# Optimization experiments

Hardware: AMD Instinct MI355X
Metric: run time of the kernel (lower is better)

## Reference

```python
import jax, jax.numpy as jnp
import numpy as np

N = 100000
E = 1600000
D_IN = 128
D_OUT = 128
D_DEC = 2
TAU = 0.5
NEG_SLOPE = 0.2  # PyG GATv2Conv default negative_slope


def _glorot(key, shape):
    lim = (6.0 / (shape[0] + shape[1])) ** 0.5
    return jax.random.uniform(key, shape, jnp.float32, -lim, lim)


def gatv2(x, edge_index, Wl, Wr, bl, br, att, bias):
    """PyG GATv2Conv, heads=1, add_self_loops=True, eval mode (no dropout).
    out[i] = sum_j softmax_i( att . leaky_relu(xl[j] + xr[i]) ) * xl[j] + bias
    """
    n = x.shape[0]
    loops = jnp.arange(n, dtype=edge_index.dtype)
    src = jnp.concatenate([edge_index[0], loops])  # [E+N]
    dst = jnp.concatenate([edge_index[1], loops])
    xl = x @ Wl + bl  # [N, out]
    xr = x @ Wr + br
    # per-edge unnormalized score
    e = jax.nn.leaky_relu(xl[src] + xr[dst], NEG_SLOPE) @ att  # [E+N]
    # scatter-softmax over incoming edges of each target node
    m = jax.ops.segment_max(e, dst, num_segments=n)
    a = jnp.exp(e - m[dst])
    s = jax.ops.segment_sum(a, dst, num_segments=n)
    alpha = a / (s[dst] + 1e-16)
    out = jax.ops.segment_sum(alpha[:, None] * xl[src], dst, num_segments=n)
    return out + bias


def setup_inputs() -> dict:
    key = jax.random.key(0)
    ks = jax.random.split(key, 16)
    x = jax.random.normal(ks[0], (N, D_IN), jnp.float32)
    edge_dec = jax.random.randint(ks[1], (2, E), 0, N, jnp.int64)
    edge_0 = jax.random.randint(ks[2], (2, E), 0, N, jnp.int64)
    edge_1 = jax.random.randint(ks[3], (2, E), 0, N, jnp.int64)
    u = jax.random.uniform(ks[4], (N, D_DEC), jnp.float32, 1e-6, 1.0 - 1e-6)
    gumbel = -jnp.log(-jnp.log(u))  # Gumbel(0,1) noise
    # shared GAT (used for every decision branch)
    Wl_g = _glorot(ks[5], (D_IN, D_OUT))
    Wr_g = _glorot(ks[6], (D_IN, D_OUT))
    bl_g = jnp.zeros((D_OUT,), jnp.float32)
    br_g = jnp.zeros((D_OUT,), jnp.float32)
    att_g = _glorot(ks[7], (D_OUT, 1))[:, 0]
    bias_g = jnp.zeros((D_OUT,), jnp.float32)
    # decision GAT
    Wl_d = _glorot(ks[8], (D_IN, D_DEC))
    Wr_d = _glorot(ks[9], (D_IN, D_DEC))
    bl_d = jnp.zeros((D_DEC,), jnp.float32)
    br_d = jnp.zeros((D_DEC,), jnp.float32)
    att_d = _glorot(ks[10], (D_DEC, 1))[:, 0]
    bias_d = jnp.zeros((D_DEC,), jnp.float32)
    return {"x": x, "edge_dec": edge_dec, "edge_0": edge_0, "edge_1": edge_1,
            "gumbel": gumbel,
            "Wl_g": Wl_g, "Wr_g": Wr_g, "bl_g": bl_g, "br_g": br_g,
            "att_g": att_g, "bias_g": bias_g,
            "Wl_d": Wl_d, "Wr_d": Wr_d, "bl_d": bl_d, "br_d": br_d,
            "att_d": att_d, "bias_d": bias_d}


def reference(x, edge_dec, edge_0, edge_1, gumbel,
              Wl_g, Wr_g, bl_g, br_g, att_g, bias_g,
              Wl_d, Wr_d, bl_d, br_d, att_d, bias_d):
    # decision logits via decision GAT on the decision edge set
    logits = gatv2(x, edge_dec, Wl_d, Wr_d, bl_d, br_d, att_d, bias_d)  # [N, 2]
    # hard gumbel-softmax with straight-through estimator, tau=0.5
    y_soft = jax.nn.softmax((logits + gumbel) / TAU, axis=-1)
    idx = jnp.argmax(y_soft, axis=-1)
    y_hard = jax.nn.one_hot(idx, y_soft.shape[-1], dtype=y_soft.dtype)
    decisions = y_hard + y_soft - jax.lax.stop_gradient(y_soft)
    # per-decision GAT (shared weights, different edge sets), gated sum
    out = jnp.zeros((x.shape[0], Wl_g.shape[1]), x.dtype)
    for i, ei in enumerate([edge_0, edge_1]):
        out = out + gatv2(x, ei, Wl_g, Wr_g, bl_g, br_g, att_g, bias_g) * decisions[:, i:i + 1]
    return out
```

## Files before the change

kernel.cpp:

```cpp
#include <hip/hip_runtime.h>

#define NEG 0.2f
#define CAPD16 384
#define CAPC16 704
#define CH 9216
#define NT 512
#define CSH 9
#define FPC 32
#define NCMAX 256
#define CHB 512
#define CCAPD 9216
#define CCAPC 17408

typedef __attribute__((ext_vector_type(8))) short short8;
typedef __attribute__((ext_vector_type(4))) float f32x4;

static __device__ __forceinline__ unsigned short f2bf(float f) {
  unsigned u = __float_as_uint(f);
  u += 0x7fffu + ((u >> 16) & 1u);
  return (unsigned short)(u >> 16);
}
static __device__ __forceinline__ float bflo(unsigned u) {
  return __uint_as_float(u << 16);
}
static __device__ __forceinline__ float bfhi(unsigned u) {
  return __uint_as_float(u & 0xffff0000u);
}
static __device__ __forceinline__ float bfx(const uint4& v, int f) {
  unsigned c = (f < 2) ? v.x : (f < 4) ? v.y : (f < 6) ? v.z : v.w;
  return (f & 1) ? bfhi(c) : bflo(c);
}
static __device__ __forceinline__ unsigned f2u(float f) {
  unsigned b = __float_as_uint(f);
  return (b & 0x80000000u) ? ~b : (b | 0x80000000u);
}
static __device__ __forceinline__ float u2f(unsigned u) {
  unsigned b = (u & 0x80000000u) ? (u ^ 0x80000000u) : ~u;
  return __uint_as_float(b);
}

__global__ void k_prep_wt(const float* __restrict__ Wl, const float* __restrict__ Wr,
                          unsigned short* __restrict__ wt, int* __restrict__ gccur,
                          int ncur) {
  if (blockIdx.x < 128) {
    int idx = blockIdx.x * 256 + threadIdx.x;
    int c = idx >> 7, k = idx & 127;
    float v = (c < 128) ? Wl[(size_t)k * 128 + c] : Wr[(size_t)k * 128 + (c - 128)];
    wt[idx] = f2bf(v);
  } else {
    int i = (blockIdx.x - 128) * 256 + threadIdx.x;
    if (i < ncur) gccur[i] = 0;
  }
}

__global__ __launch_bounds__(256) void k_gemm_main(
    const float* __restrict__ x, const unsigned short* __restrict__ wt,
    const float* __restrict__ bl, const float* __restrict__ br,
    const float* __restrict__ Wld, const float* __restrict__ Wrd,
    const float* __restrict__ bld, const float* __restrict__ brd,
    unsigned short* __restrict__ xl, unsigned short* __restrict__ xr,
    float* __restrict__ xld, float* __restrict__ xrd, int N) {
  int w = threadIdx.x >> 6, lane = threadIdx.x & 63;
  int m = lane & 15, quad = lane >> 4;
  int rowbase = blockIdx.x * 16;
  if (rowbase >= N) return;
  int colbase = w * 64;
  f32x4 acc[4] = {};
  float dl0 = 0.f, dl1 = 0.f, dr0 = 0.f, dr1 = 0.f;
  const float* arow = x + (size_t)(rowbase + m) * 128 + quad * 8;
#pragma unroll
  for (int kb = 0; kb < 128; kb += 32) {
    float4 a0 = *(const float4*)(arow + kb);
    float4 a1 = *(const float4*)(arow + kb + 4);
    if (w == 0) {
      int k0 = kb + quad * 8;
      const float4* wl4 = (const float4*)(Wld + 2 * k0);
      const float4* wr4 = (const float4*)(Wrd + 2 * k0);
      float4 l0 = wl4[0], l1 = wl4[1], l2 = wl4[2], l3 = wl4[3];
      float4 r0 = wr4[0], r1 = wr4[1], r2 = wr4[2], r3 = wr4[3];
      dl0 = fmaf(a0.x, l0.x, dl0); dl1 = fmaf(a0.x, l0.y, dl1);
      dl0 = fmaf(a0.y, l0.z, dl0); dl1 = fmaf(a0.y, l0.w, dl1);
      dl0 = fmaf(a0.z, l1.x, dl0); dl1 = fmaf(a0.z, l1.y, dl1);
      dl0 = fmaf(a0.w, l1.z, dl0); dl1 = fmaf(a0.w, l1.w, dl1);
      dl0 = fmaf(a1.x, l2.x, dl0); dl1 = fmaf(a1.x, l2.y, dl1);
      dl0 = fmaf(a1.y, l2.z, dl0); dl1 = fmaf(a1.y, l2.w, dl1);
      dl0 = fmaf(a1.z, l3.x, dl0); dl1 = fmaf(a1.z, l3.y, dl1);
      dl0 = fmaf(a1.w, l3.z, dl0); dl1 = fmaf(a1.w, l3.w, dl1);
      dr0 = fmaf(a0.x, r0.x, dr0); dr1 = fmaf(a0.x, r0.y, dr1);
      dr0 = fmaf(a0.y, r0.z, dr0); dr1 = fmaf(a0.y, r0.w, dr1);
      dr0 = fmaf(a0.z, r1.x, dr0); dr1 = fmaf(a0.z, r1.y, dr1);
      dr0 = fmaf(a0.w, r1.z, dr0); dr1 = fmaf(a0.w, r1.w, dr1);
      dr0 = fmaf(a1.x, r2.x, dr0); dr1 = fmaf(a1.x, r2.y, dr1);
      dr0 = fmaf(a1.y, r2.z, dr0); dr1 = fmaf(a1.y, r2.w, dr1);
      dr0 = fmaf(a1.z, r3.x, dr0); dr1 = fmaf(a1.z, r3.y, dr1);
      dr0 = fmaf(a1.w, r3.z, dr0); dr1 = fmaf(a1.w, r3.w, dr1);
    }
    short8 af;
    af[0] = (short)f2bf(a0.x); af[1] = (short)f2bf(a0.y);
    af[2] = (short)f2bf(a0.z); af[3] = (short)f2bf(a0.w);
    af[4] = (short)f2bf(a1.x); af[5] = (short)f2bf(a1.y);
    af[6] = (short)f2bf(a1.z); af[7] = (short)f2bf(a1.w);
#pragma unroll
    for (int ct = 0; ct < 4; ct++) {
      const unsigned short* bp =
          wt + (size_t)(colbase + ct * 16 + m) * 128 + kb + quad * 8;
      short8 bfr = *(const short8*)bp;
      acc[ct] = __builtin_amdgcn_mfma_f32_16x16x32_bf16(af, bfr, acc[ct], 0, 0, 0);
    }
  }
  if (w == 0) {
    dl0 += __shfl_xor(dl0, 16); dl0 += __shfl_xor(dl0, 32);
    dl1 += __shfl_xor(dl1, 16); dl1 += __shfl_xor(dl1, 32);
    dr0 += __shfl_xor(dr0, 16); dr0 += __shfl_xor(dr0, 32);
    dr1 += __shfl_xor(dr1, 16); dr1 += __shfl_xor(dr1, 32);
    if (quad == 0) {
      int row = rowbase + m;
      float2 vl; vl.x = dl0 + bld[0]; vl.y = dl1 + bld[1];
      float2 vr; vr.x = dr0 + brd[0]; vr.y = dr1 + brd[1];
      *(float2*)(xld + 2 * (size_t)row) = vl;
      *(float2*)(xrd + 2 * (size_t)row) = vr;
    }
  }
#pragma unroll
  for (int ct = 0; ct < 4; ct++) {
    int c = colbase + ct * 16 + m;
    float badd = (c < 128) ? bl[c] : br[c - 128];
#pragma unroll
    for (int r = 0; r < 4; r++) {
      int row = rowbase + quad * 4 + r;
      unsigned short v = f2bf(acc[ct][r] + badd);
      if (c < 128) xl[(size_t)row * 128 + c] = v;
      else         xr[(size_t)row * 128 + (c - 128)] = v;
    }
  }
}

__global__ __launch_bounds__(NT) void k_bin_coarse(
    const int* __restrict__ ed, const int* __restrict__ e0,
    const int* __restrict__ e1, int* __restrict__ gccur,
    unsigned* __restrict__ cbind, unsigned* __restrict__ cbinc,
    long E, int NC) {
  __shared__ unsigned stage[CH];
  __shared__ int h[CHB + 1];
  __shared__ int gbase[CHB];
  __shared__ int wtot[8], wexcl[8];
  int tid = threadIdx.x;
  long base = (long)blockIdx.x * CH;
  long T = 3 * E;
  for (int a = tid; a < CHB + 1; a += NT) h[a] = 0;
  __syncthreads();
  for (int it = 0; it < CH / NT; it++) {
    long idx = base + it * NT + tid;
    if (idx < T) {
      int ha;
      if (idx < E) ha = ed[E + idx] >> CSH;
      else if (idx < 2 * E) ha = NCMAX + (e0[idx] >> CSH);
      else ha = NCMAX + (e1[idx - E] >> CSH);
      atomicAdd(&h[ha], 1);
    }
  }
  __syncthreads();
  {
    int v = h[tid];
    int lane = tid & 63, wv = tid >> 6;
    int inc = v;
    for (int off = 1; off < 64; off <<= 1) {
      int nv = __shfl_up(inc, off);
      if (lane >= off) inc += nv;
    }
    if (lane == 63) wtot[wv] = inc;
    __syncthreads();
    if (tid == 0) {
      int r = 0;
      for (int i = 0; i < 8; i++) { wexcl[i] = r; r += wtot[i]; }
    }
    __syncthreads();
    int excl = wexcl[wv] + inc - v;
    h[tid] = excl;
    if (tid == NT - 1) h[CHB] = excl + v;
  }
  __syncthreads();
  {
    int a = tid;
    int cnt = h[a + 1] - h[a];
    if (cnt > 0) {
      if (a < NCMAX) { if (a < NC) gbase[a] = atomicAdd(&gccur[a], cnt); }
      else { int b = a - NCMAX; if (b < NC) gbase[a] = atomicAdd(&gccur[NC + b], cnt); }
    }
  }
  __syncthreads();
  for (int it = 0; it < CH / NT; it++) {
    long idx = base + it * NT + tid;
    if (idx < T) {
      int ha; unsigned pay;
      if (idx < E) {
        int s = ed[idx], t = ed[E + idx];
        ha = t >> CSH;
        pay = ((unsigned)s << CSH) | (unsigned)(t & ((1 << CSH) - 1));
      } else {
        int k = idx >= 2 * E;
        const int* L = k ? e1 : e0;
        long j = idx - E - (k ? E : 0);
        int s = L[j], t = L[E + j];
        ha = NCMAX + (t >> CSH);
        pay = ((unsigned)s << (CSH + 1)) | ((unsigned)k << CSH) |
              (unsigned)(t & ((1 << CSH) - 1));
      }
      int pos = atomicAdd(&h[ha], 1);
      stage[pos] = pay;
    }
  }
  __syncthreads();
  int lane = tid & 63, wv = tid >> 6;
  for (int a = wv; a < 2 * NCMAX; a += 8) {
    int start = a ? h[a - 1] : 0;
    int end = h[a];
    int len = end - start;
    if (len <= 0) continue;
    int gb = gbase[a];
    if (a < NCMAX) {
      if (a < NC) {
        unsigned* dst = cbind + (size_t)a * CCAPD;
        for (int i = lane; i < len; i += 64) {
          int o = gb + i;
          if (o < CCAPD) dst[o] = stage[start + i];
        }
      }
    } else {
      int b = a - NCMAX;
      if (b < NC) {
        unsigned* dst = cbinc + (size_t)b * CCAPC;
        for (int i = lane; i < len; i += 64) {
          int o = gb + i;
          if (o < CCAPC) dst[o] = stage[start + i];
        }
      }
    }
  }
}

__global__ __launch_bounds__(NT) void k_bin_fine(
    const unsigned* __restrict__ cbind, const unsigned* __restrict__ cbinc,
    const int* __restrict__ gccur, unsigned* __restrict__ bind,
    unsigned* __restrict__ binc, int* __restrict__ cntd, int* __restrict__ cntc,
    int NC, int NB16) {
  __shared__ int cur[FPC];
  int cb = blockIdx.x;
  int isC = cb >= NC;
  int c = isC ? cb - NC : cb;
  int cnt = gccur[cb];
  int ccap = isC ? CCAPC : CCAPD;
  if (cnt > ccap) cnt = ccap;
  const unsigned* src = isC ? (cbinc + (size_t)c * CCAPC)
                            : (cbind + (size_t)c * CCAPD);
  int tid = threadIdx.x;
  if (tid < FPC) cur[tid] = 0;
  __syncthreads();
  if (isC) {
    for (int i = tid; i < cnt; i += NT) {
      unsigned pay = src[i];
      int f = (pay >> 4) & (FPC - 1);
      int fb = c * FPC + f;
      int pos = atomicAdd(&cur[f], 1);
      unsigned o = ((pay >> (CSH + 1)) << 5) | (((pay >> CSH) & 1u) << 4) |
                   (pay & 15u);
      if (pos < CAPC16 && fb < NB16) binc[(size_t)fb * CAPC16 + pos] = o;
    }
  } else {
    for (int i = tid; i < cnt; i += NT) {
      unsigned pay = src[i];
      int f = (pay >> 4) & (FPC - 1);
      int fb = c * FPC + f;
      int pos = atomicAdd(&cur[f], 1);
      unsigned o = ((pay >> CSH) << 4) | (pay & 15u);
      if (pos < CAPD16 && fb < NB16) bind[(size_t)fb * CAPD16 + pos] = o;
    }
  }
  __syncthreads();
  if (tid < FPC) {
    int fb = c * FPC + tid;
    if (fb < NB16) {
      if (isC) { int v = cur[tid]; if (v > CAPC16) v = CAPC16; cntc[fb] = v; }
      else     { int v = cur[tid]; if (v > CAPD16) v = CAPD16; cntd[fb] = v; }
    }
  }
}

__global__ __launch_bounds__(256) void k_fused(
    const unsigned* __restrict__ bind, const unsigned* __restrict__ binc,
    const int* __restrict__ cntd_, const int* __restrict__ cntc_,
    const unsigned short* __restrict__ xl, const unsigned short* __restrict__ xr,
    const float* __restrict__ xld, const float* __restrict__ xrd,
    const float* __restrict__ attd, const float* __restrict__ biasd,
    const float* __restrict__ g, const float* __restrict__ att,
    const float* __restrict__ bias, float* __restrict__ out, int N) {
  __shared__ float xrd_s[32];
  __shared__ unsigned nmax[16];
  __shared__ float nsum[16], na0[16], na1[16];
  __shared__ int dec_s[16], scnt[16];
  __shared__ int slots[16 * 65];
  int tid = threadIdx.x;
  int b = blockIdx.x, nb0 = b << 4;
  int cdn = cntd_[b]; if (cdn > CAPD16) cdn = CAPD16;
  int ccn = cntc_[b]; if (ccn > CAPC16) ccn = CAPC16;
  float a0 = attd[0], a1 = attd[1];
  float eself = 0.f, x0s = 0.f, x1s = 0.f;
  if (tid < 16) {
    int node = nb0 + tid;
    if (node < N) {
      float2 xrv = *(const float2*)(xrd + 2 * (size_t)node);
      xrd_s[2 * tid] = xrv.x; xrd_s[2 * tid + 1] = xrv.y;
      float2 xlv = *(const float2*)(xld + 2 * (size_t)node);
      x0s = xlv.x; x1s = xlv.y;
      float h0 = x0s + xrv.x, h1 = x1s + xrv.y;
      eself = a0 * fmaxf(h0, NEG * h0) + a1 * fmaxf(h1, NEG * h1);
      nmax[tid] = f2u(eself);
    } else {
      xrd_s[2 * tid] = 0.f; xrd_s[2 * tid + 1] = 0.f;
      nmax[tid] = f2u(0.f);
    }
    nsum[tid] = 0.f; na0[tid] = 0.f; na1[tid] = 0.f;
  }
  __syncthreads();
  const unsigned* bd = bind + (size_t)b * CAPD16;
  const float2* xld2 = (const float2*)xld;
  auto dscore = [&](float2 v, int tl) {
    float h0 = v.x + xrd_s[2 * tl], h1 = v.y + xrd_s[2 * tl + 1];
    return a0 * fmaxf(h0, NEG * h0) + a1 * fmaxf(h1, NEG * h1);
  };
  for (int i = tid; i < cdn; i += 256) {
    unsigned pk = bd[i];
    float2 v = xld2[pk >> 4];
    int tl = pk & 15;
    atomicMax(&nmax[tl], f2u(dscore(v, tl)));
  }
  __syncthreads();
  for (int i = tid; i < cdn; i += 256) {
    unsigned pk = bd[i];
    float2 v = xld2[pk >> 4];
    int tl = pk & 15;
    float w = expf(dscore(v, tl) - u2f(nmax[tl]));
    atomicAdd(&nsum[tl], w); atomicAdd(&na0[tl], w * v.x); atomicAdd(&na1[tl], w * v.y);
  }
  __syncthreads();
  if (tid < 16) {
    int node = nb0 + tid;
    if (node < N) {
      float mm = u2f(nmax[tid]);
      float ws = expf(eself - mm);
      float den = nsum[tid] + ws + 1e-16f;
      float z0 = (na0[tid] + ws * x0s) / den + biasd[0] + g[2 * (size_t)node];
      float z1 = (na1[tid] + ws * x1s) / den + biasd[1] + g[2 * (size_t)node + 1];
      dec_s[tid] = (z1 > z0) ? 1 : 0;
      scnt[tid] = 1; slots[tid * 65] = node;
    } else {
      dec_s[tid] = -1; scnt[tid] = 0; slots[tid * 65] = 0;
    }
  }
  __syncthreads();
  const unsigned* bc = binc + (size_t)b * CAPC16;
  for (int i = tid; i < ccn; i += 256) {
    unsigned pk = bc[i];
    int tl = pk & 15, k = (pk >> 4) & 1;
    if (k == dec_s[tl]) {
      int pos = atomicAdd(&scnt[tl], 1);
      if (pos < 64) slots[tl * 65 + pos] = pk >> 5;
    }
  }
  __syncthreads();

  int l = tid & 15, gg = tid >> 4;
  const float4* at4 = (const float4*)att;
  float4 atA = at4[l * 2], atB = at4[l * 2 + 1];
  float atv[8] = {atA.x, atA.y, atA.z, atA.w, atB.x, atB.y, atB.z, atB.w};
  const float4* b4 = (const float4*)bias;
  float4 bA = b4[l * 2], bB = b4[l * 2 + 1];

  int nd = nb0 + gg;
  bool nvalid = nd < N;
  int cnt = scnt[gg]; if (cnt > 64) cnt = 64;
  if (!nvalid) cnt = 0;
  int mc = max(cnt, __shfl_xor(cnt, 16));
  mc = max(mc, __shfl_xor(mc, 32));

  int nc = nvalid ? nd : 0;
  uint4 xrp = ((const uint4*)(xr + (size_t)nc * 128))[l];
  float xrv[8] = {bflo(xrp.x), bfhi(xrp.x), bflo(xrp.y), bfhi(xrp.y),
                  bflo(xrp.z), bfhi(xrp.z), bflo(xrp.w), bfhi(xrp.w)};

  int cl = cnt - 1; if (cl < 0) cl = 0;
  const int* srow = &slots[gg * 65];
  uint4 cur[4];
#pragma unroll
  for (int j = 0; j < 4; j++) {
    int idx = j > cl ? cl : j;
    cur[j] = ((const uint4*)(xl + (size_t)srow[idx] * 128))[l];
  }
  float m = -3.0e38f, lsum = 0.f;
  float gacc[8] = {0.f, 0.f, 0.f, 0.f, 0.f, 0.f, 0.f, 0.f};

  for (int e = 0; e < mc; e += 4) {
    uint4 nxt[4];
#pragma unroll
    for (int j = 0; j < 4; j++) {
      int idx = e + 4 + j; if (idx > cl) idx = cl;
      nxt[j] = ((const uint4*)(xl + (size_t)srow[idx] * 128))[l];
    }
    float p[4];
#pragma unroll
    for (int j = 0; j < 4; j++) {
      float pj = 0.f;
#pragma unroll
      for (int f = 0; f < 8; f++) {
        float h = bfx(cur[j], f) + xrv[f];
        pj = fmaf(atv[f], fmaxf(h, NEG * h), pj);
      }
      p[j] = pj;
    }
#pragma unroll
    for (int off = 1; off < 16; off <<= 1) {
      p[0] += __shfl_xor(p[0], off); p[1] += __shfl_xor(p[1], off);
      p[2] += __shfl_xor(p[2], off); p[3] += __shfl_xor(p[3], off);
    }
    float pe0 = (e     < cnt) ? p[0] : -3.0e38f;
    float pe1 = (e + 1 < cnt) ? p[1] : -3.0e38f;
    float pe2 = (e + 2 < cnt) ? p[2] : -3.0e38f;
    float pe3 = (e + 3 < cnt) ? p[3] : -3.0e38f;
    float nm = fmaxf(m, fmaxf(fmaxf(pe0, pe1), fmaxf(pe2, pe3)));
    float sc = __expf(m - nm);
    float w0 = __expf(pe0 - nm), w1 = __expf(pe1 - nm);
    float w2 = __expf(pe2 - nm), w3 = __expf(pe3 - nm);
    lsum = lsum * sc + w0 + w1 + w2 + w3;
#pragma unroll
    for (int f = 0; f < 8; f++) {
      float t0 = fmaf(w0, bfx(cur[0], f), gacc[f] * sc);
      float t1 = fmaf(w1, bfx(cur[1], f), t0);
      float t2 = fmaf(w2, bfx(cur[2], f), t1);
      gacc[f]  = fmaf(w3, bfx(cur[3], f), t2);
    }
    m = nm;
#pragma unroll
    for (int j = 0; j < 4; j++) cur[j] = nxt[j];
  }
  if (nvalid) {
    float inv = 1.0f / (lsum + 1e-16f);
    float4 oA, oB;
    oA.x = gacc[0] * inv + bA.x; oA.y = gacc[1] * inv + bA.y;
    oA.z = gacc[2] * inv + bA.z; oA.w = gacc[3] * inv + bA.w;
    oB.x = gacc[4] * inv + bB.x; oB.y = gacc[5] * inv + bB.y;
    oB.z = gacc[6] * inv + bB.z; oB.w = gacc[7] * inv + bB.w;
    float4* op = (float4*)(out + (size_t)nd * 128 + l * 8);
    op[0] = oA; op[1] = oB;
  }
}

extern "C" void kernel_launch(void* const* d_in, const int* in_sizes, int n_in,
                              void* d_out, int out_size, void* d_ws, size_t ws_size,
                              hipStream_t stream) {
  const float* x      = (const float*)d_in[0];
  const int*   ed     = (const int*)d_in[1];
  const int*   e0     = (const int*)d_in[2];
  const int*   e1     = (const int*)d_in[3];
  const float* gumbel = (const float*)d_in[4];
  const float* Wl_g   = (const float*)d_in[5];
  const float* Wr_g   = (const float*)d_in[6];
  const float* bl_g   = (const float*)d_in[7];
  const float* br_g   = (const float*)d_in[8];
  const float* att_g  = (const float*)d_in[9];
  const float* bias_g = (const float*)d_in[10];
  const float* Wl_d   = (const float*)d_in[11];
  const float* Wr_d   = (const float*)d_in[12];
  const float* bl_d   = (const float*)d_in[13];
  const float* br_d   = (const float*)d_in[14];
  const float* att_d  = (const float*)d_in[15];
  const float* bias_d = (const float*)d_in[16];

  const int  N    = in_sizes[0] / 128;
  const long E    = in_sizes[1] / 2;
  const int  NB16 = (N + 15) / 16;
  const int  NC   = (N + (1 << CSH) - 1) >> CSH;

  char* p = (char*)d_ws;
  auto alloc = [&](size_t bytes) -> void* {
    void* r = (void*)p;
    p += (bytes + 255) & ~(size_t)255;
    return r;
  };
  unsigned short* xl = (unsigned short*)alloc((size_t)N * 128 * 2);
  unsigned short* xr = (unsigned short*)alloc((size_t)N * 128 * 2);
  unsigned short* wt = (unsigned short*)alloc((size_t)256 * 128 * 2);
  float* xld      = (float*)alloc((size_t)N * 2 * 4);
  float* xrd      = (float*)alloc((size_t)N * 2 * 4);
  int* gccur      = (int*)alloc((size_t)2 * NC * 4);
  int* cntd       = (int*)alloc((size_t)NB16 * 4);
  int* cntc       = (int*)alloc((size_t)NB16 * 4);
  unsigned* bind  = (unsigned*)alloc((size_t)NB16 * CAPD16 * 4);
  unsigned* binc  = (unsigned*)alloc((size_t)NB16 * CAPC16 * 4);
  unsigned* cbind = (unsigned*)xl;
  unsigned* cbinc = (unsigned*)xr;

  const int gB = (int)((3 * E + CH - 1) / CH);
  const int gZ = (2 * NC + 255) / 256;

  k_prep_wt<<<128 + gZ, 256, 0, stream>>>(Wl_g, Wr_g, wt, gccur, 2 * NC);
  k_bin_coarse<<<gB, NT, 0, stream>>>(ed, e0, e1, gccur, cbind, cbinc, E, NC);
  k_bin_fine<<<2 * NC, NT, 0, stream>>>(cbind, cbinc, gccur, bind, binc,
                                        cntd, cntc, NC, NB16);
  k_gemm_main<<<(N + 15) / 16, 256, 0, stream>>>(x, wt, bl_g, br_g, Wl_d, Wr_d,
                                                 bl_d, br_d, xl, xr, xld, xrd, N);
  k_fused<<<NB16, 256, 0, stream>>>(bind, binc, cntd, cntc, xl, xr, xld, xrd,
                                    att_d, bias_d, gumbel, att_g, bias_g,
                                    (float*)d_out, N);
}
```

Baseline: 396.8 us.

## Split leaky_relu score into linear per-node terms plus abs, widen edge batch to 8

Uses leaky_relu(h) = 0.6h + 0.4|h| to precompute per-node linear attention terms (0.6·att·xl, 0.6·att·xr) in the GEMM epilogue. The edge loop then only evaluates 0.4·att·|h| and adds the precomputed scalars, replacing a max and a multiply with an abs. The aggregation loop now processes and prefetches 8 neighbours per iteration instead of 4, and occupancy is hinted with launch_bounds(256,4). This costs an extra per-edge scalar gather, more registers and a small shared-memory reduction in the GEMM.

```diff
diff --git a/kernel.cpp b/kernel.cpp
--- a/kernel.cpp
+++ b/kernel.cpp
@@ -58,8 +58,11 @@
     const float* __restrict__ bl, const float* __restrict__ br,
     const float* __restrict__ Wld, const float* __restrict__ Wrd,
     const float* __restrict__ bld, const float* __restrict__ brd,
+    const float* __restrict__ att,
     unsigned short* __restrict__ xl, unsigned short* __restrict__ xr,
-    float* __restrict__ xld, float* __restrict__ xrd, int N) {
+    float* __restrict__ xld, float* __restrict__ xrd,
+    float* __restrict__ al6, float* __restrict__ ar6, int N) {
+  __shared__ float alr_s[2][16];
   int w = threadIdx.x >> 6, lane = threadIdx.x & 63;
   int m = lane & 15, quad = lane >> 4;
   int rowbase = blockIdx.x * 16;
@@ -121,18 +124,36 @@
       *(float2*)(xrd + 2 * (size_t)row) = vr;
     }
   }
+  if (threadIdx.x < 32) alr_s[threadIdx.x >> 4][threadIdx.x & 15] = 0.f;
+  __syncthreads();
+  float part[4] = {0.f, 0.f, 0.f, 0.f};
 #pragma unroll
   for (int ct = 0; ct < 4; ct++) {
     int c = colbase + ct * 16 + m;
     float badd = (c < 128) ? bl[c] : br[c - 128];
+    float av = 0.6f * ((c < 128) ? att[c] : att[c - 128]);
 #pragma unroll
     for (int r = 0; r < 4; r++) {
       int row = rowbase + quad * 4 + r;
       unsigned short v = f2bf(acc[ct][r] + badd);
       if (c < 128) xl[(size_t)row * 128 + c] = v;
       else         xr[(size_t)row * 128 + (c - 128)] = v;
-    }
-  }
+      part[r] = fmaf(av, __uint_as_float((unsigned)v << 16), part[r]);
+    }
+  }
+#pragma unroll
+  for (int off = 1; off < 16; off <<= 1) {
+#pragma unroll
+    for (int r = 0; r < 4; r++) part[r] += __shfl_xor(part[r], off);
+  }
+  if (m == 0) {
+#pragma unroll
+    for (int r = 0; r < 4; r++)
+      atomicAdd(&alr_s[w >> 1][quad * 4 + r], part[r]);
+  }
+  __syncthreads();
+  if (threadIdx.x < 16) al6[rowbase + threadIdx.x] = alr_s[0][threadIdx.x];
+  else if (threadIdx.x < 32) ar6[rowbase + threadIdx.x - 16] = alr_s[1][threadIdx.x - 16];
 }
 
 __global__ __launch_bounds__(NT) void k_bin_coarse(
@@ -286,13 +307,14 @@
   }
 }
 
-__global__ __launch_bounds__(256) void k_fused(
+__global__ __launch_bounds__(256, 4) void k_fused(
     const unsigned* __restrict__ bind, const unsigned* __restrict__ binc,
     const int* __restrict__ cntd_, const int* __restrict__ cntc_,
     const unsigned short* __restrict__ xl, const unsigned short* __restrict__ xr,
     const float* __restrict__ xld, const float* __restrict__ xrd,
     const float* __restrict__ attd, const float* __restrict__ biasd,
     const float* __restrict__ g, const float* __restrict__ att,
+    const float* __restrict__ al6, const float* __restrict__ ar6,
     const float* __restrict__ bias, float* __restrict__ out, int N) {
   __shared__ float xrd_s[32];
   __shared__ unsigned nmax[16];
@@ -372,9 +394,8 @@
   int l = tid & 15, gg = tid >> 4;
   const float4* at4 = (const float4*)att;
   float4 atA = at4[l * 2], atB = at4[l * 2 + 1];
-  float atv[8] = {atA.x, atA.y, atA.z, atA.w, atB.x, atB.y, atB.z, atB.w};
-  const float4* b4 = (const float4*)bias;
-  float4 bA = b4[l * 2], bB = b4[l * 2 + 1];
+  float atv[8] = {0.4f * atA.x, 0.4f * atA.y, 0.4f * atA.z, 0.4f * atA.w,
+                  0.4f * atB.x, 0.4f * atB.y, 0.4f * atB.z, 0.4f * atB.w};
 
   int nd = nb0 + gg;
   bool nvalid = nd < N;
@@ -387,62 +408,72 @@
   uint4 xrp = ((const uint4*)(xr + (size_t)nc * 128))[l];
   float xrv[8] = {bflo(xrp.x), bfhi(xrp.x), bflo(xrp.y), bfhi(xrp.y),
                   bflo(xrp.z), bfhi(xrp.z), bflo(xrp.w), bfhi(xrp.w)};
+  float art = ar6[nc];
 
   int cl = cnt - 1; if (cl < 0) cl = 0;
   const int* srow = &slots[gg * 65];
-  uint4 cur[4];
-#pragma unroll
-  for (int j = 0; j < 4; j++) {
+  uint4 cur[8]; float alc[8];
+#pragma unroll
+  for (int j = 0; j < 8; j++) {
     int idx = j > cl ? cl : j;
-    cur[j] = ((const uint4*)(xl + (size_t)srow[idx] * 128))[l];
+    int s = srow[idx];
+    cur[j] = ((const uint4*)(xl + (size_t)s * 128))[l];
+    alc[j] = al6[s];
   }
   float m = -3.0e38f, lsum = 0.f;
   float gacc[8] = {0.f, 0.f, 0.f, 0.f, 0.f, 0.f, 0.f, 0.f};
 
-  for (int e = 0; e < mc; e += 4) {
-    uint4 nxt[4];
-#pragma unroll
-    for (int j = 0; j < 4; j++) {
-      int idx = e + 4 + j; if (idx > cl) idx = cl;
-      nxt[j] = ((const uint4*)(xl + (size_t)srow[idx] * 128))[l];
-    }
-    float p[4];
-#pragma unroll
-    for (int j = 0; j < 4; j++) {
+  for (int e = 0; e < mc; e += 8) {
+    uint4 nxt[8]; float aln[8];
+#pragma unroll
+    for (int j = 0; j < 8; j++) {
+      int idx = e + 8 + j; if (idx > cl) idx = cl;
+      int s = srow[idx];
+      nxt[j] = ((const uint4*)(xl + (size_t)s * 128))[l];
+      aln[j] = al6[s];
+    }
+    float p[8];
+#pragma unroll
+    for (int j = 0; j < 8; j++) {
       float pj = 0.f;
 #pragma unroll
       for (int f = 0; f < 8; f++) {
         float h = bfx(cur[j], f) + xrv[f];
-        pj = fmaf(atv[f], fmaxf(h, NEG * h), pj);
+        pj = fmaf(atv[f], fabsf(h), pj);
       }
       p[j] = pj;
     }
 #pragma unroll
     for (int off = 1; off < 16; off <<= 1) {
-      p[0] += __shfl_xor(p[0], off); p[1] += __shfl_xor(p[1], off);
-      p[2] += __shfl_xor(p[2], off); p[3] += __shfl_xor(p[3], off);
-    }
-    float pe0 = (e     < cnt) ? p[0] : -3.0e38f;
-    float pe1 = (e + 1 < cnt) ? p[1] : -3.0e38f;
-    float pe2 = (e + 2 < cnt) ? p[2] : -3.0e38f;
-    float pe3 = (e + 3 < cnt) ? p[3] : -3.0e38f;
-    float nm = fmaxf(m, fmaxf(fmaxf(pe0, pe1), fmaxf(pe2, pe3)));
+#pragma unroll
+      for (int j = 0; j < 8; j++) p[j] += __shfl_xor(p[j], off);
+    }
+#pragma unroll
+    for (int j = 0; j < 8; j++) {
+      float pf = p[j] + alc[j] + art;
+      p[j] = (e + j < cnt) ? pf : -3.0e38f;
+    }
+    float nm = m;
+#pragma unroll
+    for (int j = 0; j < 8; j++) nm = fmaxf(nm, p[j]);
     float sc = __expf(m - nm);
-    float w0 = __expf(pe0 - nm), w1 = __expf(pe1 - nm);
-    float w2 = __expf(pe2 - nm), w3 = __expf(pe3 - nm);
-    lsum = lsum * sc + w0 + w1 + w2 + w3;
-#pragma unroll
-    for (int f = 0; f < 8; f++) {
-      float t0 = fmaf(w0, bfx(cur[0], f), gacc[f] * sc);
-      float t1 = fmaf(w1, bfx(cur[1], f), t0);
-      float t2 = fmaf(w2, bfx(cur[2], f), t1);
-      gacc[f]  = fmaf(w3, bfx(cur[3], f), t2);
+    lsum *= sc;
+#pragma unroll
+    for (int f = 0; f < 8; f++) gacc[f] *= sc;
+#pragma unroll
+    for (int j = 0; j < 8; j++) {
+      float w = __expf(p[j] - nm);
+      lsum += w;
+#pragma unroll
+      for (int f = 0; f < 8; f++) gacc[f] = fmaf(w, bfx(cur[j], f), gacc[f]);
     }
     m = nm;
 #pragma unroll
-    for (int j = 0; j < 4; j++) cur[j] = nxt[j];
+    for (int j = 0; j < 8; j++) { cur[j] = nxt[j]; alc[j] = aln[j]; }
   }
   if (nvalid) {
+    const float4* b4 = (const float4*)bias;
+    float4 bA = b4[l * 2], bB = b4[l * 2 + 1];
     float inv = 1.0f / (lsum + 1e-16f);
     float4 oA, oB;
     oA.x = gacc[0] * inv + bA.x; oA.y = gacc[1] * inv + bA.y;
@@ -491,6 +522,8 @@
   unsigned short* wt = (unsigned short*)alloc((size_t)256 * 128 * 2);
   float* xld      = (float*)alloc((size_t)N * 2 * 4);
   float* xrd      = (float*)alloc((size_t)N * 2 * 4);
+  float* al6      = (float*)alloc((size_t)N * 4);
+  float* ar6      = (float*)alloc((size_t)N * 4);
   int* gccur      = (int*)alloc((size_t)2 * NC * 4);
   int* cntd       = (int*)alloc((size_t)NB16 * 4);
   int* cntc       = (int*)alloc((size_t)NB16 * 4);
@@ -507,8 +540,9 @@
   k_bin_fine<<<2 * NC, NT, 0, stream>>>(cbind, cbinc, gccur, bind, binc,
                                         cntd, cntc, NC, NB16);
   k_gemm_main<<<(N + 15) / 16, 256, 0, stream>>>(x, wt, bl_g, br_g, Wl_d, Wr_d,
-                                                 bl_d, br_d, xl, xr, xld, xrd, N);
+                                                 bl_d, br_d, att_g, xl, xr,
+                                                 xld, xrd, al6, ar6, N);
   k_fused<<<NB16, 256, 0, stream>>>(bind, binc, cntd, cntc, xl, xr, xld, xrd,
-                                    att_d, bias_d, gumbel, att_g, bias_g,
-                                    (float*)d_out, N);
-}
+                                    att_d, bias_d, gumbel, att_g, al6, ar6,
+                                    bias_g, (float*)d_out, N);
+}
```

New measurement: 409.5 us. +3.2%, slower.
